# Kernel tuning notes

Measured on AMD Instinct MI355X. Metric: run time of the kernel, lower is better.

## Reference

```python
import jax, jax.numpy as jnp
import numpy as np

B, S, D_MODEL, NHEAD = 1, 512, 512, 8
D_K = D_MODEL // NHEAD
EPS = 1e-6


def _linear(x, w, b):
    # torch nn.Linear: x @ W^T + b
    return x @ w.T + b


def setup_inputs() -> dict:
    key = jax.random.key(0)
    ks = jax.random.split(key, 18)
    inp = {}
    for i, nm in enumerate(["query", "key", "value", "query_sigma", "key_sigma", "value_sigma"]):
        inp[nm] = jax.random.normal(ks[i], (B, S, D_MODEL), dtype=jnp.float32)
    bound = 1.0 / np.sqrt(D_MODEL)
    pnames = ["wq_mu", "bq_mu", "wk_mu", "bk_mu", "wv_mu", "bv_mu",
              "wq_s", "bq_s", "wk_s", "bk_s", "wv_s", "bv_s"]
    for i, nm in enumerate(pnames):
        shape = (D_MODEL, D_MODEL) if nm.startswith("w") else (D_MODEL,)
        inp[nm] = jax.random.uniform(ks[6 + i], shape, dtype=jnp.float32,
                                     minval=-bound, maxval=bound)
    return inp


def reference(query, key, value, query_sigma, key_sigma, value_sigma,
              wq_mu, bq_mu, wk_mu, bk_mu, wv_mu, bv_mu,
              wq_s, bq_s, wk_s, bk_s, wv_s, bv_s):
    b, s, _ = query.shape
    h, dk = NHEAD, D_K
    mu_q = _linear(query, wq_mu, bq_mu).reshape(b, s, h, dk)
    mu_k = _linear(key, wk_mu, bk_mu).reshape(b, s, h, dk)
    mu_v = _linear(value, wv_mu, bv_mu).reshape(b, s, h, dk)
    sg_q = _linear(query_sigma, wq_s, bq_s).reshape(b, s, h, dk)
    sg_k = _linear(key_sigma, wk_s, bk_s).reshape(b, s, h, dk)
    sg_v = _linear(value_sigma, wv_s, bv_s).reshape(b, s, h, dk)

    # Bhattacharyya distance: broadcast to [b, s_q, s_k, h, dk] then reduce dk
    a = sg_q[:, :, None] ** 2 + EPS   # [b, sq, 1, h, dk]
    c = sg_k[:, None, :] ** 2 + EPS   # [b, 1, sk, h, dk]
    term1 = 0.25 * jnp.log(0.25 * (a / c + c / a + 2.0))
    dmu = mu_q[:, :, None] - mu_k[:, None, :]
    term2 = 0.25 * dmu ** 2 / (sg_q[:, :, None] ** 2 + sg_k[:, None, :] ** 2 + EPS)
    dist = (term1 + term2).sum(-1) / np.sqrt(dk)  # [b, sq, sk, h]
    dist = dist.transpose(0, 3, 1, 2)             # [b, h, sq, sk]

    causal = jnp.triu(jnp.ones((s, s), dtype=bool), k=1)
    dist = jnp.where(causal[None, None], -jnp.inf, dist)
    attn = jax.nn.softmax(dist, axis=-1)

    out_mu = jnp.einsum('bhqk,bkhd->bhqd', attn, mu_v)
    out_var = jnp.maximum(jnp.einsum('bhqk,bkhd->bhqd', attn, sg_v ** 2), 0.0)
    out_sigma = jnp.sqrt(out_var + EPS)
    return out_mu, out_sigma
```

## Files before the change

kernel.cpp:

```cpp
#include <hip/hip_runtime.h>
#include <hip/hip_bf16.h>
#include <math.h>

#define SEQ 512
#define DM 512
#define NH 8
#define DKH 64
#define EPSV 1e-6f
#define LN2F 0.6931471805599453f

typedef __attribute__((ext_vector_type(8))) short short8v;
typedef __attribute__((ext_vector_type(8))) unsigned short ushort8v;
typedef __attribute__((ext_vector_type(16))) float f32x16;

__device__ inline unsigned short f2bf(float x) {
  union { float f; unsigned u; } v; v.f = x;
  unsigned r = v.u + 0x7FFFu + ((v.u >> 16) & 1u);
  return (unsigned short)(r >> 16);
}
__device__ inline float bf2f(unsigned short h) {
  union { float f; unsigned u; } v; v.u = ((unsigned)h) << 16;
  return v.f;
}

struct ConvArgs { const float* src[12]; };

__global__ __launch_bounds__(256) void convert_kernel(ConvArgs a,
                                                      unsigned short* __restrict__ pack) {
  const int m = blockIdx.x >> 7;
  const int g = ((blockIdx.x & 127) << 8) + threadIdx.x;
  const int r = g & 31, ko = (g >> 5) & 63, p = g >> 11;
  const float* src = a.src[m] + (p * 32 + r) * DM + ko * 8;
  float4 x0 = *(const float4*)src;
  float4 x1 = *(const float4*)(src + 4);
  float xs[8] = {x0.x, x0.y, x0.z, x0.w, x1.x, x1.y, x1.z, x1.w};
  ushort8v h1, h2, h3;
#pragma unroll
  for (int e = 0; e < 8; ++e) {
    unsigned short a1 = f2bf(xs[e]);
    float r1 = xs[e] - bf2f(a1);
    unsigned short a2 = f2bf(r1);
    float r2 = r1 - bf2f(a2);
    h1[e] = a1; h2[e] = a2; h3[e] = f2bf(r2);
  }
  unsigned short* dh = pack + (size_t)m * 786432 + p * 16384 + ko * 256 + r * 8;
  *(ushort8v*)dh = h1;
  *(ushort8v*)(dh + 262144) = h2;
  *(ushort8v*)(dh + 524288) = h3;
}

struct GemmArgs { const float* bias[6]; float* out[6]; };

__global__ __launch_bounds__(512) void mfma_proj_kernel(const unsigned short* __restrict__ pack,
                                                        GemmArgs ga) {
  const int p = blockIdx.z;
  const int by = blockIdx.y, bx = blockIdx.x;
  const int t = threadIdx.x, l = t & 63, w = t >> 6;
  const int qd = w & 3, kh = w >> 2;
  const int rowblk = qd >> 1, colblk = qd & 1;
  const int r = l & 31, koff = l >> 5;

  const unsigned short* A = pack + (size_t)p * 786432;
  const unsigned short* B = pack + (size_t)(6 + p) * 786432;
  const int pa = by * 2 + rowblk, pb = bx * 2 + colblk;
  const int ko0 = kh * 32 + koff;
  const size_t aoff = (size_t)pa * 16384 + (size_t)ko0 * 256 + r * 8;
  const size_t boff = (size_t)pb * 16384 + (size_t)ko0 * 256 + r * 8;
  const short8v* A1 = (const short8v*)(A + aoff);
  const short8v* A2 = (const short8v*)(A + 262144 + aoff);
  const short8v* A3 = (const short8v*)(A + 524288 + aoff);
  const short8v* B1 = (const short8v*)(B + boff);
  const short8v* B2 = (const short8v*)(B + 262144 + boff);
  const short8v* B3 = (const short8v*)(B + 524288 + boff);

  f32x16 acc = {};
#pragma unroll 2
  for (int s = 0; s < 16; ++s) {
    short8v a1 = A1[(size_t)s * 64];
    short8v a2 = A2[(size_t)s * 64];
    short8v a3 = A3[(size_t)s * 64];
    short8v b1 = B1[(size_t)s * 64];
    short8v b2 = B2[(size_t)s * 64];
    short8v b3 = B3[(size_t)s * 64];
    acc = __builtin_amdgcn_mfma_f32_32x32x16_bf16(a1, b1, acc, 0, 0, 0);
    acc = __builtin_amdgcn_mfma_f32_32x32x16_bf16(a2, b1, acc, 0, 0, 0);
    acc = __builtin_amdgcn_mfma_f32_32x32x16_bf16(a1, b2, acc, 0, 0, 0);
    acc = __builtin_amdgcn_mfma_f32_32x32x16_bf16(a3, b1, acc, 0, 0, 0);
    acc = __builtin_amdgcn_mfma_f32_32x32x16_bf16(a2, b2, acc, 0, 0, 0);
    acc = __builtin_amdgcn_mfma_f32_32x32x16_bf16(a1, b3, acc, 0, 0, 0);
  }

  __shared__ float red[4][32][33];
  if (kh == 1) {
#pragma unroll
    for (int i = 0; i < 16; ++i) {
      int row = (i & 3) + 8 * (i >> 2) + 4 * (l >> 5);
      red[qd][row][r] = acc[i];
    }
  }
  __syncthreads();
  if (kh == 0) {
    const int colg = bx * 64 + colblk * 32 + r;
    const float bias = ga.bias[p][colg];
    float* C = ga.out[p];
    const int rowbase = by * 64 + rowblk * 32;
#pragma unroll
    for (int i = 0; i < 16; ++i) {
      int row = (i & 3) + 8 * (i >> 2) + 4 * (l >> 5);
      float v = acc[i] + red[qd][row][r] + bias;
      if (p >= 3) v = fmaf(v, v, (p == 5) ? 0.f : EPSV);
      C[(size_t)(rowbase + row) * DM + colg] = v;
    }
  }
}

__global__ __launch_bounds__(256) void dist_kernel(const float* __restrict__ aq,
                                                   const float* __restrict__ ak,
                                                   const float* __restrict__ mq,
                                                   const float* __restrict__ mk,
                                                   float* __restrict__ dist) {
  const int blk = blockIdx.x;
  const int h = blk / 72;
  const int tt = blk % 72;
  int qt = (int)sqrtf((float)tt);
  while ((qt + 1) * (qt + 2) <= tt) ++qt;
  while (qt * (qt + 1) > tt) --qt;
  const int kt = tt - qt * (qt + 1);

  __shared__ float aqs[64][68], mqs[64][68], aks[32][68], mks[32][68];
  __shared__ float lsum[96][2];
  const int t = threadIdx.x;
#pragma unroll
  for (int i = 0; i < 4; ++i) {
    int idx = t + 256 * i;
    int r = idx >> 4, c4 = idx & 15;
    int gq = (qt * 64 + r) * DM + h * 64 + c4 * 4;
    *(float4*)&aqs[r][c4 * 4] = *(const float4*)&aq[gq];
    *(float4*)&mqs[r][c4 * 4] = *(const float4*)&mq[gq];
  }
#pragma unroll
  for (int i = 0; i < 2; ++i) {
    int idx = t + 256 * i;
    int r = idx >> 4, c4 = idx & 15;
    int gk = (kt * 32 + r) * DM + h * 64 + c4 * 4;
    *(float4*)&aks[r][c4 * 4] = *(const float4*)&ak[gk];
    *(float4*)&mks[r][c4 * 4] = *(const float4*)&mk[gk];
  }
  __syncthreads();

  if (t < 192) {
    int row = t >> 1, par = t & 1;
    const float* src = (row < 64) ? &aqs[row][0] : &aks[row - 64][0];
    float s = 0.f;
#pragma unroll
    for (int d = 0; d < 32; d += 4) {
      float pr = src[par * 32 + d] * src[par * 32 + d + 1]
               * src[par * 32 + d + 2] * src[par * 32 + d + 3];
      s += __log2f(pr);
    }
    lsum[row][par] = s;
  }
  __syncthreads();

  const int tq = t >> 4, tk = t & 15;
  float accl[4][2], acct[4][2];
#pragma unroll
  for (int i = 0; i < 4; ++i)
#pragma unroll
    for (int j = 0; j < 2; ++j) { accl[i][j] = 0.f; acct[i][j] = 0.f; }

#pragma unroll 2
  for (int d4 = 0; d4 < 16; ++d4) {
    float4 qa[4], qm[4], ka[2], km[2];
#pragma unroll
    for (int i = 0; i < 4; ++i) {
      qa[i] = *(const float4*)&aqs[tq * 4 + i][d4 * 4];
      qm[i] = *(const float4*)&mqs[tq * 4 + i][d4 * 4];
    }
#pragma unroll
    for (int j = 0; j < 2; ++j) {
      ka[j] = *(const float4*)&aks[tk + 16 * j][d4 * 4];
      km[j] = *(const float4*)&mks[tk + 16 * j][d4 * 4];
    }
#pragma unroll
    for (int i = 0; i < 4; ++i) {
      float qav[4] = {qa[i].x, qa[i].y, qa[i].z, qa[i].w};
      float qmv[4] = {qm[i].x, qm[i].y, qm[i].z, qm[i].w};
#pragma unroll
      for (int j = 0; j < 2; ++j) {
        float kav[4] = {ka[j].x, ka[j].y, ka[j].z, ka[j].w};
        float kmv[4] = {km[j].x, km[j].y, km[j].z, km[j].w};
        float pr = 1.f;
#pragma unroll
        for (int e = 0; e < 4; ++e) {
          float s = qav[e] + kav[e];
          pr = (e == 0) ? s : pr * s;
          float dm = qmv[e] - kmv[e];
          float rcp = __builtin_amdgcn_rcpf(s - EPSV);
          acct[i][j] = fmaf(dm * dm, rcp, acct[i][j]);
        }
        accl[i][j] += __log2f(pr);
      }
    }
  }

  const int qg0 = qt * 64 + tq * 4;
#pragma unroll
  for (int i = 0; i < 4; ++i) {
    float la2 = lsum[tq * 4 + i][0] + lsum[tq * 4 + i][1];
#pragma unroll
    for (int j = 0; j < 2; ++j) {
      int kg = kt * 32 + tk + 16 * j;
      float lc2 = lsum[64 + tk + 16 * j][0] + lsum[64 + tk + 16 * j][1];
      float dv = (LN2F * (0.5f * accl[i][j] - 0.25f * (la2 + lc2) - 32.f)
                  + 0.25f * acct[i][j]) * 0.125f;
      dist[((size_t)(h * SEQ) + qg0 + i) * SEQ + kg] = dv;
    }
  }
}

__global__ __launch_bounds__(256) void softmax_pvpack_kernel(const float* __restrict__ dist,
                                                             const float* __restrict__ mv,
                                                             const float* __restrict__ sv2,
                                                             unsigned short* __restrict__ aPack,
                                                             unsigned short* __restrict__ vPack) {
  __shared__ float tile[64][65];
  const int t = threadIdx.x;

  if (blockIdx.x < 1024) {
    const int wid = blockIdx.x * 4 + (t >> 6);
    const int l = t & 63;
    const int h = wid >> 9;
    const int q = wid & 511;
    const float* row = dist + (size_t)wid * SEQ;

    float vals[8];
    float m = -1e30f;
    if (l * 8 <= q) {
      float4 v0 = *(const float4*)&row[l * 8];
      float4 v1 = *(const float4*)&row[l * 8 + 4];
      vals[0] = v0.x; vals[1] = v0.y; vals[2] = v0.z; vals[3] = v0.w;
      vals[4] = v1.x; vals[5] = v1.y; vals[6] = v1.z; vals[7] = v1.w;
#pragma unroll
      for (int e = 0; e < 8; ++e) {
        vals[e] = (l * 8 + e <= q) ? vals[e] : -1e30f;
        m = fmaxf(m, vals[e]);
      }
    } else {
#pragma unroll
      for (int e = 0; e < 8; ++e) vals[e] = -1e30f;
    }
#pragma unroll
    for (int o = 32; o; o >>= 1) m = fmaxf(m, __shfl_xor(m, o, 64));
    float ssum = 0.f;
#pragma unroll
    for (int e = 0; e < 8; ++e) {
      float p = (l * 8 + e <= q) ? __expf(vals[e] - m) : 0.f;
      vals[e] = p;
      ssum += p;
    }
#pragma unroll
    for (int o = 32; o; o >>= 1) ssum += __shfl_xor(ssum, o, 64);
    float rs = 1.f / ssum;

    ushort8v hi;
#pragma unroll
    for (int e = 0; e < 8; ++e) hi[e] = f2bf(vals[e] * rs);
    unsigned short* dst = aPack + (size_t)h * 262144 + (q >> 5) * 16384 + l * 256 + (q & 31) * 8;
    *(ushort8v*)dst = hi;
  } else {
    const int bb = blockIdx.x - 1024;
    const int h = bb >> 1;
    const int mm = bb & 1;
    const float* src = (mm == 0) ? mv : sv2;
    unsigned short* base = vPack + (size_t)(h * 2 + mm) * 65536;

    for (int k0 = 0; k0 < SEQ; k0 += 64) {
      __syncthreads();
#pragma unroll
      for (int i = 0; i < 4; ++i) {
        int idx = t + 256 * i;
        int r = idx >> 4, c4 = idx & 15;
        float4 v = *(const float4*)&src[(size_t)(k0 + r) * DM + h * 64 + c4 * 4];
        tile[r][c4 * 4 + 0] = v.x; tile[r][c4 * 4 + 1] = v.y;
        tile[r][c4 * 4 + 2] = v.z; tile[r][c4 * 4 + 3] = v.w;
      }
      __syncthreads();
#pragma unroll
      for (int i = 0; i < 2; ++i) {
        int idx = t + 256 * i;
        int d = idx & 63, ko = idx >> 6;
        ushort8v hi, lo;
#pragma unroll
        for (int e = 0; e < 8; ++e) {
          float x = tile[ko * 8 + e][d];
          unsigned short hh = f2bf(x);
          hi[e] = hh;
          lo[e] = f2bf(x - bf2f(hh));
        }
        int koG = (k0 >> 3) + ko;
        unsigned short* dst = base + (d >> 5) * 16384 + koG * 256 + (d & 31) * 8;
        *(ushort8v*)dst = hi;
        *(ushort8v*)(dst + 32768) = lo;
      }
    }
  }
}

__global__ __launch_bounds__(256) void pv_mfma_kernel(const unsigned short* __restrict__ aPack,
                                                      const unsigned short* __restrict__ vPack,
                                                      float* __restrict__ out) {
  const int h = blockIdx.x >> 4;
  const int qt = blockIdx.x & 15;
  const int t = threadIdx.x, l = t & 63, w = t >> 6;
  const int dt = w & 1, mm = w >> 1;

  const unsigned short* aBase = aPack + (size_t)h * 262144 + qt * 16384
                                + (l >> 5) * 256 + (l & 31) * 8;
  const unsigned short* vBase = vPack + (size_t)(h * 2 + mm) * 65536 + dt * 16384
                                + (l >> 5) * 256 + (l & 31) * 8;

  f32x16 acc = {};
  const int nks = 2 * qt + 2;
#pragma unroll 2
  for (int s = 0; s < nks; ++s) {
    short8v a1 = *(const short8v*)(aBase + (size_t)s * 512);
    short8v b1 = *(const short8v*)(vBase + (size_t)s * 512);
    short8v b2 = *(const short8v*)(vBase + 32768 + (size_t)s * 512);
    acc = __builtin_amdgcn_mfma_f32_32x32x16_bf16(a1, b1, acc, 0, 0, 0);
    acc = __builtin_amdgcn_mfma_f32_32x32x16_bf16(a1, b2, acc, 0, 0, 0);
  }

  float* dst = out + ((mm == 0) ? 0 : (size_t)NH * SEQ * DKH);
  const int col = dt * 32 + (l & 31);
#pragma unroll
  for (int i = 0; i < 16; ++i) {
    int qrow = (i & 3) + 8 * (i >> 2) + 4 * (l >> 5);
    int q = qt * 32 + qrow;
    float v = acc[i];
    if (mm) v = sqrtf(fmaxf(v, 0.f) + EPSV);
    dst[((size_t)h * SEQ + q) * DKH + col] = v;
  }
}

extern "C" void kernel_launch(void* const* d_in, const int* in_sizes, int n_in,
                              void* d_out, int out_size, void* d_ws, size_t ws_size,
                              hipStream_t stream) {
  (void)in_sizes; (void)n_in; (void)out_size; (void)ws_size;

  float* ws = (float*)d_ws;
  float* mq = ws;
  float* mk = mq + 262144;
  float* mv = mk + 262144;
  float* sq = mv + 262144;
  float* sk = sq + 262144;
  float* sv = sk + 262144;
  unsigned short* pack = (unsigned short*)(sv + 262144);
  float* dist = (float*)pack;
  unsigned short* aPack = pack + 4194304;
  unsigned short* vPack = pack + 6291456;

  ConvArgs ca;
  ca.src[0] = (const float*)d_in[0];
  ca.src[1] = (const float*)d_in[1];
  ca.src[2] = (const float*)d_in[2];
  ca.src[3] = (const float*)d_in[3];
  ca.src[4] = (const float*)d_in[4];
  ca.src[5] = (const float*)d_in[5];
  ca.src[6] = (const float*)d_in[6];
  ca.src[7] = (const float*)d_in[8];
  ca.src[8] = (const float*)d_in[10];
  ca.src[9] = (const float*)d_in[12];
  ca.src[10] = (const float*)d_in[14];
  ca.src[11] = (const float*)d_in[16];

  GemmArgs gaArgs;
  gaArgs.bias[0] = (const float*)d_in[7];  gaArgs.out[0] = mq;
  gaArgs.bias[1] = (const float*)d_in[9];  gaArgs.out[1] = mk;
  gaArgs.bias[2] = (const float*)d_in[11]; gaArgs.out[2] = mv;
  gaArgs.bias[3] = (const float*)d_in[13]; gaArgs.out[3] = sq;
  gaArgs.bias[4] = (const float*)d_in[15]; gaArgs.out[4] = sk;
  gaArgs.bias[5] = (const float*)d_in[17]; gaArgs.out[5] = sv;

  convert_kernel<<<12 * 128, 256, 0, stream>>>(ca, pack);

  dim3 ggrid(8, 8, 6);
  mfma_proj_kernel<<<ggrid, 512, 0, stream>>>(pack, gaArgs);

  dist_kernel<<<8 * 72, 256, 0, stream>>>(sq, sk, mq, mk, dist);

  softmax_pvpack_kernel<<<1040, 256, 0, stream>>>(dist, mv, sv, aPack, vPack);

  pv_mfma_kernel<<<128, 256, 0, stream>>>(aPack, vPack, (float*)d_out);
}
```

Before: 159.8 us.

## Fuse V packing into projection epilogue and use two-level split for V

The value projections (mu_v and sigma_v squared) now write their bf16 hi/lo packed layout straight from the GEMM epilogue, instead of going through fp32 buffers that a separate softmax-side block then repacked. Those two projections also use a 3-MFMA two-level split in place of the 6-MFMA three-level one, and the convert kernel skips writing their third residual level. The PV kernel is split into 256 blocks of 128 threads for more parallelism. The cost is a small precision reduction for the V projections and a relocated vPack buffer in the workspace.

```diff
diff --git a/kernel.cpp b/kernel.cpp
--- a/kernel.cpp
+++ b/kernel.cpp
@@ -11,6 +11,7 @@
 
 typedef __attribute__((ext_vector_type(8))) short short8v;
 typedef __attribute__((ext_vector_type(8))) unsigned short ushort8v;
+typedef __attribute__((ext_vector_type(4))) unsigned short ushort4v;
 typedef __attribute__((ext_vector_type(16))) float f32x16;
 
 __device__ inline unsigned short f2bf(float x) {
@@ -46,10 +47,11 @@
   unsigned short* dh = pack + (size_t)m * 786432 + p * 16384 + ko * 256 + r * 8;
   *(ushort8v*)dh = h1;
   *(ushort8v*)(dh + 262144) = h2;
-  *(ushort8v*)(dh + 524288) = h3;
-}
-
-struct GemmArgs { const float* bias[6]; float* out[6]; };
+  const bool two_level = (m == 2) || (m == 5) || (m == 8) || (m == 11);
+  if (!two_level) *(ushort8v*)(dh + 524288) = h3;
+}
+
+struct GemmArgs { const float* bias[6]; float* out[6]; unsigned short* vPack; };
 
 __global__ __launch_bounds__(512) void mfma_proj_kernel(const unsigned short* __restrict__ pack,
                                                         GemmArgs ga) {
@@ -73,21 +75,35 @@
   const short8v* B2 = (const short8v*)(B + 262144 + boff);
   const short8v* B3 = (const short8v*)(B + 524288 + boff);
 
+  const bool lite = (p == 2) || (p == 5);
   f32x16 acc = {};
+  if (lite) {
 #pragma unroll 2
-  for (int s = 0; s < 16; ++s) {
-    short8v a1 = A1[(size_t)s * 64];
-    short8v a2 = A2[(size_t)s * 64];
-    short8v a3 = A3[(size_t)s * 64];
-    short8v b1 = B1[(size_t)s * 64];
-    short8v b2 = B2[(size_t)s * 64];
-    short8v b3 = B3[(size_t)s * 64];
-    acc = __builtin_amdgcn_mfma_f32_32x32x16_bf16(a1, b1, acc, 0, 0, 0);
-    acc = __builtin_amdgcn_mfma_f32_32x32x16_bf16(a2, b1, acc, 0, 0, 0);
-    acc = __builtin_amdgcn_mfma_f32_32x32x16_bf16(a1, b2, acc, 0, 0, 0);
-    acc = __builtin_amdgcn_mfma_f32_32x32x16_bf16(a3, b1, acc, 0, 0, 0);
-    acc = __builtin_amdgcn_mfma_f32_32x32x16_bf16(a2, b2, acc, 0, 0, 0);
-    acc = __builtin_amdgcn_mfma_f32_32x32x16_bf16(a1, b3, acc, 0, 0, 0);
+    for (int s = 0; s < 16; ++s) {
+      short8v a1 = A1[(size_t)s * 64];
+      short8v a2 = A2[(size_t)s * 64];
+      short8v b1 = B1[(size_t)s * 64];
+      short8v b2 = B2[(size_t)s * 64];
+      acc = __builtin_amdgcn_mfma_f32_32x32x16_bf16(a1, b1, acc, 0, 0, 0);
+      acc = __builtin_amdgcn_mfma_f32_32x32x16_bf16(a2, b1, acc, 0, 0, 0);
+      acc = __builtin_amdgcn_mfma_f32_32x32x16_bf16(a1, b2, acc, 0, 0, 0);
+    }
+  } else {
+#pragma unroll 2
+    for (int s = 0; s < 16; ++s) {
+      short8v a1 = A1[(size_t)s * 64];
+      short8v a2 = A2[(size_t)s * 64];
+      short8v a3 = A3[(size_t)s * 64];
+      short8v b1 = B1[(size_t)s * 64];
+      short8v b2 = B2[(size_t)s * 64];
+      short8v b3 = B3[(size_t)s * 64];
+      acc = __builtin_amdgcn_mfma_f32_32x32x16_bf16(a1, b1, acc, 0, 0, 0);
+      acc = __builtin_amdgcn_mfma_f32_32x32x16_bf16(a2, b1, acc, 0, 0, 0);
+      acc = __builtin_amdgcn_mfma_f32_32x32x16_bf16(a1, b2, acc, 0, 0, 0);
+      acc = __builtin_amdgcn_mfma_f32_32x32x16_bf16(a3, b1, acc, 0, 0, 0);
+      acc = __builtin_amdgcn_mfma_f32_32x32x16_bf16(a2, b2, acc, 0, 0, 0);
+      acc = __builtin_amdgcn_mfma_f32_32x32x16_bf16(a1, b3, acc, 0, 0, 0);
+    }
   }
 
   __shared__ float red[4][32][33];
@@ -102,14 +118,36 @@
   if (kh == 0) {
     const int colg = bx * 64 + colblk * 32 + r;
     const float bias = ga.bias[p][colg];
-    float* C = ga.out[p];
     const int rowbase = by * 64 + rowblk * 32;
-#pragma unroll
-    for (int i = 0; i < 16; ++i) {
-      int row = (i & 3) + 8 * (i >> 2) + 4 * (l >> 5);
-      float v = acc[i] + red[qd][row][r] + bias;
-      if (p >= 3) v = fmaf(v, v, (p == 5) ? 0.f : EPSV);
-      C[(size_t)(rowbase + row) * DM + colg] = v;
+    if (lite) {
+      const int mm = (p == 5);
+      unsigned short* vb = ga.vPack + (size_t)(bx * 2 + mm) * 65536
+                         + colblk * 16384 + (rowbase >> 3) * 256 + r * 8 + (l >> 5) * 4;
+#pragma unroll
+      for (int g = 0; g < 4; ++g) {
+        ushort4v hi4, lo4;
+#pragma unroll
+        for (int e = 0; e < 4; ++e) {
+          int i = g * 4 + e;
+          int row = (i & 3) + 8 * (i >> 2) + 4 * (l >> 5);
+          float v = acc[i] + red[qd][row][r] + bias;
+          if (p == 5) v = v * v;
+          unsigned short hh = f2bf(v);
+          hi4[e] = hh;
+          lo4[e] = f2bf(v - bf2f(hh));
+        }
+        *(ushort4v*)(vb + g * 256) = hi4;
+        *(ushort4v*)(vb + 32768 + g * 256) = lo4;
+      }
+    } else {
+      float* C = ga.out[p];
+#pragma unroll
+      for (int i = 0; i < 16; ++i) {
+        int row = (i & 3) + 8 * (i >> 2) + 4 * (l >> 5);
+        float v = acc[i] + red[qd][row][r] + bias;
+        if (p >= 3) v = fmaf(v, v, EPSV);
+        C[(size_t)(rowbase + row) * DM + colg] = v;
+      }
     }
   }
 }
@@ -219,101 +257,60 @@
   }
 }
 
-__global__ __launch_bounds__(256) void softmax_pvpack_kernel(const float* __restrict__ dist,
-                                                             const float* __restrict__ mv,
-                                                             const float* __restrict__ sv2,
-                                                             unsigned short* __restrict__ aPack,
-                                                             unsigned short* __restrict__ vPack) {
-  __shared__ float tile[64][65];
+__global__ __launch_bounds__(256) void softmax_kernel(const float* __restrict__ dist,
+                                                      unsigned short* __restrict__ aPack) {
   const int t = threadIdx.x;
-
-  if (blockIdx.x < 1024) {
-    const int wid = blockIdx.x * 4 + (t >> 6);
-    const int l = t & 63;
-    const int h = wid >> 9;
-    const int q = wid & 511;
-    const float* row = dist + (size_t)wid * SEQ;
-
-    float vals[8];
-    float m = -1e30f;
-    if (l * 8 <= q) {
-      float4 v0 = *(const float4*)&row[l * 8];
-      float4 v1 = *(const float4*)&row[l * 8 + 4];
-      vals[0] = v0.x; vals[1] = v0.y; vals[2] = v0.z; vals[3] = v0.w;
-      vals[4] = v1.x; vals[5] = v1.y; vals[6] = v1.z; vals[7] = v1.w;
-#pragma unroll
-      for (int e = 0; e < 8; ++e) {
-        vals[e] = (l * 8 + e <= q) ? vals[e] : -1e30f;
-        m = fmaxf(m, vals[e]);
-      }
-    } else {
-#pragma unroll
-      for (int e = 0; e < 8; ++e) vals[e] = -1e30f;
-    }
-#pragma unroll
-    for (int o = 32; o; o >>= 1) m = fmaxf(m, __shfl_xor(m, o, 64));
-    float ssum = 0.f;
+  const int wid = blockIdx.x * 4 + (t >> 6);
+  const int l = t & 63;
+  const int h = wid >> 9;
+  const int q = wid & 511;
+  const float* row = dist + (size_t)wid * SEQ;
+
+  float vals[8];
+  float m = -1e30f;
+  if (l * 8 <= q) {
+    float4 v0 = *(const float4*)&row[l * 8];
+    float4 v1 = *(const float4*)&row[l * 8 + 4];
+    vals[0] = v0.x; vals[1] = v0.y; vals[2] = v0.z; vals[3] = v0.w;
+    vals[4] = v1.x; vals[5] = v1.y; vals[6] = v1.z; vals[7] = v1.w;
 #pragma unroll
     for (int e = 0; e < 8; ++e) {
-      float p = (l * 8 + e <= q) ? __expf(vals[e] - m) : 0.f;
-      vals[e] = p;
-      ssum += p;
-    }
-#pragma unroll
-    for (int o = 32; o; o >>= 1) ssum += __shfl_xor(ssum, o, 64);
-    float rs = 1.f / ssum;
-
-    ushort8v hi;
-#pragma unroll
-    for (int e = 0; e < 8; ++e) hi[e] = f2bf(vals[e] * rs);
-    unsigned short* dst = aPack + (size_t)h * 262144 + (q >> 5) * 16384 + l * 256 + (q & 31) * 8;
-    *(ushort8v*)dst = hi;
+      vals[e] = (l * 8 + e <= q) ? vals[e] : -1e30f;
+      m = fmaxf(m, vals[e]);
+    }
   } else {
-    const int bb = blockIdx.x - 1024;
-    const int h = bb >> 1;
-    const int mm = bb & 1;
-    const float* src = (mm == 0) ? mv : sv2;
-    unsigned short* base = vPack + (size_t)(h * 2 + mm) * 65536;
-
-    for (int k0 = 0; k0 < SEQ; k0 += 64) {
-      __syncthreads();
-#pragma unroll
-      for (int i = 0; i < 4; ++i) {
-        int idx = t + 256 * i;
-        int r = idx >> 4, c4 = idx & 15;
-        float4 v = *(const float4*)&src[(size_t)(k0 + r) * DM + h * 64 + c4 * 4];
-        tile[r][c4 * 4 + 0] = v.x; tile[r][c4 * 4 + 1] = v.y;
-        tile[r][c4 * 4 + 2] = v.z; tile[r][c4 * 4 + 3] = v.w;
-      }
-      __syncthreads();
-#pragma unroll
-      for (int i = 0; i < 2; ++i) {
-        int idx = t + 256 * i;
-        int d = idx & 63, ko = idx >> 6;
-        ushort8v hi, lo;
-#pragma unroll
-        for (int e = 0; e < 8; ++e) {
-          float x = tile[ko * 8 + e][d];
-          unsigned short hh = f2bf(x);
-          hi[e] = hh;
-          lo[e] = f2bf(x - bf2f(hh));
-        }
-        int koG = (k0 >> 3) + ko;
-        unsigned short* dst = base + (d >> 5) * 16384 + koG * 256 + (d & 31) * 8;
-        *(ushort8v*)dst = hi;
-        *(ushort8v*)(dst + 32768) = lo;
-      }
-    }
-  }
-}
-
-__global__ __launch_bounds__(256) void pv_mfma_kernel(const unsigned short* __restrict__ aPack,
+#pragma unroll
+    for (int e = 0; e < 8; ++e) vals[e] = -1e30f;
+  }
+#pragma unroll
+  for (int o = 32; o; o >>= 1) m = fmaxf(m, __shfl_xor(m, o, 64));
+  float ssum = 0.f;
+#pragma unroll
+  for (int e = 0; e < 8; ++e) {
+    float p = (l * 8 + e <= q) ? __expf(vals[e] - m) : 0.f;
+    vals[e] = p;
+    ssum += p;
+  }
+#pragma unroll
+  for (int o = 32; o; o >>= 1) ssum += __shfl_xor(ssum, o, 64);
+  float rs = 1.f / ssum;
+
+  ushort8v hi;
+#pragma unroll
+  for (int e = 0; e < 8; ++e) hi[e] = f2bf(vals[e] * rs);
+  unsigned short* dst = aPack + (size_t)h * 262144 + (q >> 5) * 16384 + l * 256 + (q & 31) * 8;
+  *(ushort8v*)dst = hi;
+}
+
+__global__ __launch_bounds__(128) void pv_mfma_kernel(const unsigned short* __restrict__ aPack,
                                                       const unsigned short* __restrict__ vPack,
                                                       float* __restrict__ out) {
-  const int h = blockIdx.x >> 4;
-  const int qt = blockIdx.x & 15;
-  const int t = threadIdx.x, l = t & 63, w = t >> 6;
-  const int dt = w & 1, mm = w >> 1;
+  const int b = blockIdx.x;
+  const int h = b >> 5;
+  const int qt = (b >> 1) & 15;
+  const int mm = b & 1;
+  const int t = threadIdx.x, l = t & 63;
+  const int dt = t >> 6;
 
   const unsigned short* aBase = aPack + (size_t)h * 262144 + qt * 16384
                                 + (l >> 5) * 256 + (l & 31) * 8;
@@ -358,7 +355,7 @@
   unsigned short* pack = (unsigned short*)(sv + 262144);
   float* dist = (float*)pack;
   unsigned short* aPack = pack + 4194304;
-  unsigned short* vPack = pack + 6291456;
+  unsigned short* vPack = pack + 9437184;
 
   ConvArgs ca;
   ca.src[0] = (const float*)d_in[0];
@@ -381,6 +378,7 @@
   gaArgs.bias[3] = (const float*)d_in[13]; gaArgs.out[3] = sq;
   gaArgs.bias[4] = (const float*)d_in[15]; gaArgs.out[4] = sk;
   gaArgs.bias[5] = (const float*)d_in[17]; gaArgs.out[5] = sv;
+  gaArgs.vPack = vPack;
 
   convert_kernel<<<12 * 128, 256, 0, stream>>>(ca, pack);
 
@@ -389,7 +387,7 @@
 
   dist_kernel<<<8 * 72, 256, 0, stream>>>(sq, sk, mq, mk, dist);
 
-  softmax_pvpack_kernel<<<1040, 256, 0, stream>>>(dist, mv, sv, aPack, vPack);
-
-  pv_mfma_kernel<<<128, 256, 0, stream>>>(aPack, vPack, (float*)d_out);
-}
+  softmax_kernel<<<1024, 256, 0, stream>>>(dist, aPack);
+
+  pv_mfma_kernel<<<256, 128, 0, stream>>>(aPack, vPack, (float*)d_out);
+}
```

Measured after the change: 154.6 us. 3.3% less time.
